# Kernel tuning notes

Measured on AMD Instinct MI355X. Metric: run time of the kernel, lower is better.

Reference implementation:

```python
import jax, jax.numpy as jnp
import numpy as np

N_NODES = 50000
D_IN = 128
D_OUT = 128
N_EDGES = 800000


def setup_inputs() -> dict:
    key = jax.random.key(0)
    ks = jax.random.split(key, 6)
    x = jax.random.normal(ks[0], (N_NODES, D_IN), dtype=jnp.float32)
    # xavier-uniform-ish init for the per-support weights
    limit = float(np.sqrt(6.0 / (D_IN + D_OUT)))
    weights = jax.random.uniform(ks[1], (2, D_IN, D_OUT), dtype=jnp.float32,
                                 minval=-limit, maxval=limit)
    edge_idx0 = jax.random.randint(ks[2], (2, N_EDGES), 0, N_NODES, dtype=jnp.int64 if jax.config.jax_enable_x64 else jnp.int32)
    vals0 = jax.random.uniform(ks[3], (N_EDGES,), dtype=jnp.float32)
    edge_idx1 = jax.random.randint(ks[4], (2, N_EDGES), 0, N_NODES, dtype=jnp.int64 if jax.config.jax_enable_x64 else jnp.int32)
    vals1 = jax.random.uniform(ks[5], (N_EDGES,), dtype=jnp.float32)
    return {"x": x, "weights": weights, "edge_idx0": edge_idx0, "vals0": vals0,
            "edge_idx1": edge_idx1, "vals1": vals1}


def _spmm(edge_idx, vals, dense, n_rows):
    # (sparse COO A) @ dense : out[row] += vals * dense[col]
    rows, cols = edge_idx[0], edge_idx[1]
    gathered = dense[cols] * vals[:, None]  # [E, D_OUT]
    return jax.ops.segment_sum(gathered, rows, num_segments=n_rows)


def reference(x, weights, edge_idx0, vals0, edge_idx1, vals1):
    n = x.shape[0]
    out = jnp.zeros((n, D_OUT), dtype=x.dtype)
    for w, ei, v in ((weights[0], edge_idx0, vals0), (weights[1], edge_idx1, vals1)):
        pre_sup = x @ w                       # [N, D_OUT] dense GEMM
        out = out + _spmm(ei, v, pre_sup, n)  # SpMM accumulate
    return jax.nn.relu(out)
```

## Files before the change

kernel.cpp:

```cpp
#include <hip/hip_runtime.h>

#define N_NODES 50000
#define D 128
#define N_EDGES 800000
#define SCAN_BLOCKS ((N_NODES + 255) / 256)
#define GEMM_BLOCKS ((N_NODES + 63) / 64)
#define BINS 196
#define NB1 64
#define CH1 12500
#define NKEY 2048

typedef __attribute__((ext_vector_type(8))) short short8;
typedef __attribute__((ext_vector_type(4))) float f32x4;
typedef __attribute__((ext_vector_type(2))) float f32x2;

__device__ __forceinline__ unsigned short f2bf(float f) {
    unsigned u = __builtin_bit_cast(unsigned, f);
    u += 0x7FFFu + ((u >> 16) & 1u);
    return (unsigned short)(u >> 16);
}
__device__ __forceinline__ float bflo(unsigned p) {
    return __builtin_bit_cast(float, p << 16);
}
__device__ __forceinline__ float bfhi(unsigned p) {
    return __builtin_bit_cast(float, p & 0xFFFF0000u);
}

__global__ __launch_bounds__(256) void wt_build(const float* __restrict__ w,
                                                unsigned short* __restrict__ wt) {
    int i = blockIdx.x * 256 + threadIdx.x;
    if (i < 2 * D * D) {
        int s = i >> 14, rem = i & 16383, c = rem >> 7, k = rem & 127;
        wt[i] = f2bf(w[s * D * D + k * D + c]);
    }
}

template<int NS>
__device__ __forceinline__ void gemm_body(const float* __restrict__ x,
                                          const unsigned short* __restrict__ wt,
                                          unsigned short* __restrict__ pre0,
                                          unsigned short* __restrict__ pre1,
                                          int n_rows, int blk) {
    const int lane = threadIdx.x & 63;
    const int wid  = threadIdx.x >> 6;
    const int q    = lane >> 4;
    const int rlo  = lane & 15;
    const int r0   = blk * 64 + wid * 16;
    if (r0 >= n_rows) return;

    const float4* x4 = (const float4*)x;
    int arow  = r0 + rlo;
    int arowc = arow < n_rows ? arow : n_rows - 1;

    short8 afr[4];
    #pragma unroll
    for (int kb = 0; kb < 4; ++kb) {
        float4 fa = x4[(size_t)arowc * 32 + kb * 8 + q * 2];
        float4 fb = x4[(size_t)arowc * 32 + kb * 8 + q * 2 + 1];
        short8 a;
        a[0] = (short)f2bf(fa.x); a[1] = (short)f2bf(fa.y);
        a[2] = (short)f2bf(fa.z); a[3] = (short)f2bf(fa.w);
        a[4] = (short)f2bf(fb.x); a[5] = (short)f2bf(fb.y);
        a[6] = (short)f2bf(fb.z); a[7] = (short)f2bf(fb.w);
        afr[kb] = a;
    }

    const short8* wt8 = (const short8*)wt;
    f32x4 acc[NS][8];
    #pragma unroll
    for (int s = 0; s < NS; ++s)
        #pragma unroll
        for (int t = 0; t < 8; ++t)
            acc[s][t] = (f32x4){0.f, 0.f, 0.f, 0.f};

    #pragma unroll
    for (int t = 0; t < 8; ++t) {
        int c = t * 16 + rlo;
        #pragma unroll
        for (int kb = 0; kb < 4; ++kb) {
            short8 b0 = wt8[(size_t)c * 16 + kb * 4 + q];
            acc[0][t] = __builtin_amdgcn_mfma_f32_16x16x32_bf16(afr[kb], b0, acc[0][t], 0, 0, 0);
            if (NS == 2) {
                short8 b1 = wt8[(size_t)(D + c) * 16 + kb * 4 + q];
                acc[NS - 1][t] = __builtin_amdgcn_mfma_f32_16x16x32_bf16(afr[kb], b1, acc[NS - 1][t], 0, 0, 0);
            }
        }
    }

    #pragma unroll
    for (int i = 0; i < 4; ++i) {
        int rw = r0 + q * 4 + i;
        if (rw < n_rows) {
            #pragma unroll
            for (int t = 0; t < 8; ++t) {
                pre0[(size_t)rw * D + t * 16 + rlo] = f2bf(acc[0][t][i]);
                if (NS == 2) pre1[(size_t)rw * D + t * 16 + rlo] = f2bf(acc[NS - 1][t][i]);
            }
        }
    }
}


__global__ __launch_bounds__(256) void p1_count(const int* __restrict__ r0,
                                                const int* __restrict__ r1,
                                                int* __restrict__ h) {
    int s = blockIdx.y, blk = blockIdx.x;
    const int* r = s ? r1 : r0;
    __shared__ int hist[BINS];
    for (int i = threadIdx.x; i < BINS; i += 256) hist[i] = 0;
    __syncthreads();
    int start = blk * CH1, end = start + CH1;
    for (int e = start + (int)threadIdx.x; e < end; e += 256)
        atomicAdd(&hist[r[e] >> 8], 1);
    __syncthreads();
    for (int i = threadIdx.x; i < BINS; i += 256)
        h[(size_t)(s * NB1 + blk) * BINS + i] = hist[i];
}

__global__ __launch_bounds__(256) void binredscan(const int* __restrict__ h,
                                                  int* __restrict__ binbase) {
    int s = blockIdx.x, t = threadIdx.x;
    int acc[8] = {0, 0, 0, 0, 0, 0, 0, 0};
    if (t < BINS) {
        for (int blk = 0; blk < NB1; blk += 8) {
            #pragma unroll
            for (int j = 0; j < 8; ++j)
                acc[j] += h[(size_t)(s * NB1 + blk + j) * BINS + t];
        }
    }
    int v = acc[0] + acc[1] + acc[2] + acc[3] + acc[4] + acc[5] + acc[6] + acc[7];
    const int lane = t & 63, wid = t >> 6;
    __shared__ int ws[4];
    int incl = v;
    #pragma unroll
    for (int o = 1; o < 64; o <<= 1) { int tv = __shfl_up(incl, o); if (lane >= o) incl += tv; }
    if (lane == 63) ws[wid] = incl;
    __syncthreads();
    int wbase = 0;
    #pragma unroll
    for (int j = 0; j < 4; ++j) wbase += (j < wid) ? ws[j] : 0;
    int excl = wbase + incl - v;
    if (t < BINS) binbase[s * (BINS + 1) + t] = excl;
    if (t == BINS - 1) binbase[s * (BINS + 1) + BINS] = excl + v;
}

__global__ __launch_bounds__(64) void blkscan(int* __restrict__ h,
                                              const int* __restrict__ binbase) {
    int s = blockIdx.y, bin = blockIdx.x, t = threadIdx.x;
    size_t idx = (size_t)(s * NB1 + t) * BINS + bin;
    int v = h[idx];
    int incl = v;
    #pragma unroll
    for (int o = 1; o < 64; o <<= 1) { int tv = __shfl_up(incl, o); if (t >= o) incl += tv; }
    h[idx] = binbase[s * (BINS + 1) + bin] + (incl - v);
}

#define LWT_STRIDE 17
__global__ __launch_bounds__(256) void k_fill_gemm(const float* __restrict__ x,
                                                   const unsigned short* __restrict__ wt,
                                                   unsigned short* __restrict__ pre0,
                                                   unsigned short* __restrict__ pre1,
                                                   const int* __restrict__ r0, const int* __restrict__ c0,
                                                   const float* __restrict__ v0,
                                                   const int* __restrict__ r1, const int* __restrict__ c1,
                                                   const float* __restrict__ v1,
                                                   const int* __restrict__ h,
                                                   int2* __restrict__ rec, int n_rows) {
    __shared__ int base[BINS];
    __shared__ int cnt2[BINS];
    __shared__ short8 lwt[2 * D * LWT_STRIDE];
    int bid = blockIdx.x;
    if (bid < 2 * NB1) {
        int s = bid & 1, blk = bid >> 1;
        const int*   r = s ? r1 : r0;
        const int*   c = s ? c1 : c0;
        const float* v = s ? v1 : v0;
        int2* rs = rec + (size_t)s * N_EDGES;
        for (int i = threadIdx.x; i < BINS; i += 256) {
            base[i] = h[(size_t)(s * NB1 + blk) * BINS + i];
            cnt2[i] = 0;
        }
        __syncthreads();
        int start = blk * CH1, end = start + CH1;
        for (int e = start + (int)threadIdx.x; e < end; e += 256) {
            int rr = r[e], cc = c[e];
            float vv = v[e];
            int bin = rr >> 8;
            int lr = atomicAdd(&cnt2[bin], 1);
            rs[base[bin] + lr] = make_int2((cc << 8) | (rr & 255), __float_as_int(vv));
        }
    } else {
        int blk = bid - 2 * NB1;
        const short8* wg = (const short8*)wt;
        for (int i = threadIdx.x; i < 2 * D * 16; i += 256) {
            int cc = i >> 4, ee = i & 15;
            lwt[cc * LWT_STRIDE + ee] = wg[i];
        }
        __syncthreads();

        const int lane = threadIdx.x & 63;
        const int wid  = threadIdx.x >> 6;
        const int q    = lane >> 4;
        const int rlo  = lane & 15;
        const int r0g  = blk * 64 + wid * 16;
        if (r0g < n_rows) {
            const float4* x4 = (const float4*)x;
            int arow  = r0g + rlo;
            int arowc = arow < n_rows ? arow : n_rows - 1;

            short8 afr[4];
            #pragma unroll
            for (int kb = 0; kb < 4; ++kb) {
                float4 fa = x4[(size_t)arowc * 32 + kb * 8 + q * 2];
                float4 fb = x4[(size_t)arowc * 32 + kb * 8 + q * 2 + 1];
                short8 a;
                a[0] = (short)f2bf(fa.x); a[1] = (short)f2bf(fa.y);
                a[2] = (short)f2bf(fa.z); a[3] = (short)f2bf(fa.w);
                a[4] = (short)f2bf(fb.x); a[5] = (short)f2bf(fb.y);
                a[6] = (short)f2bf(fb.z); a[7] = (short)f2bf(fb.w);
                afr[kb] = a;
            }

            f32x4 acc[2][8];
            #pragma unroll
            for (int s = 0; s < 2; ++s)
                #pragma unroll
                for (int t = 0; t < 8; ++t)
                    acc[s][t] = (f32x4){0.f, 0.f, 0.f, 0.f};

            #pragma unroll
            for (int t = 0; t < 8; ++t) {
                int c = t * 16 + rlo;
                #pragma unroll
                for (int kb = 0; kb < 4; ++kb) {
                    short8 b0 = lwt[c * LWT_STRIDE + kb * 4 + q];
                    acc[0][t] = __builtin_amdgcn_mfma_f32_16x16x32_bf16(afr[kb], b0, acc[0][t], 0, 0, 0);
                    short8 b1 = lwt[(D + c) * LWT_STRIDE + kb * 4 + q];
                    acc[1][t] = __builtin_amdgcn_mfma_f32_16x16x32_bf16(afr[kb], b1, acc[1][t], 0, 0, 0);
                }
            }

            #pragma unroll
            for (int i = 0; i < 4; ++i) {
                int rw = r0g + q * 4 + i;
                if (rw < n_rows) {
                    #pragma unroll
                    for (int t = 0; t < 8; ++t) {
                        pre0[(size_t)rw * D + t * 16 + rlo] = f2bf(acc[0][t][i]);
                        pre1[(size_t)rw * D + t * 16 + rlo] = f2bf(acc[1][t][i]);
                    }
                }
            }
        }
    }
}

__global__ __launch_bounds__(512) void p2_sort(const int* __restrict__ binbase,
                                               const int2* __restrict__ rec,
                                               unsigned* __restrict__ ep,
                                               int* __restrict__ off) {
    int s = blockIdx.y, bin = blockIdx.x, t = threadIdx.x;
    int bs  = binbase[s * (BINS + 1) + bin];
    int be  = binbase[s * (BINS + 1) + bin + 1];
    int cnt = be - bs;
    const int2* rs = rec + (size_t)s * N_EDGES;
    unsigned* es = ep + (size_t)s * N_EDGES;
    __shared__ int lc[NKEY];
    __shared__ int cur[NKEY];
    __shared__ int ws[8];
    #pragma unroll
    for (int j = 0; j < NKEY / 512; ++j) lc[t + j * 512] = 0;
    __syncthreads();
    for (int i = t; i < cnt; i += 512) {
        int2 R = rs[bs + i];
        int col = R.x >> 8;
        int key = ((R.x & 255) << 3) | (col >> 13);
        atomicAdd(&lc[key], 1);
    }
    __syncthreads();
    int kb = t * 4;
    int s0 = lc[kb], s1 = lc[kb + 1], s2 = lc[kb + 2], s3 = lc[kb + 3];
    int tot = s0 + s1 + s2 + s3;
    const int lane = t & 63, wid = t >> 6;
    int incl = tot;
    #pragma unroll
    for (int o = 1; o < 64; o <<= 1) { int tv = __shfl_up(incl, o); if (lane >= o) incl += tv; }
    if (lane == 63) ws[wid] = incl;
    __syncthreads();
    int wbase = 0;
    #pragma unroll
    for (int j = 0; j < 8; ++j) wbase += (j < wid) ? ws[j] : 0;
    int excl = wbase + incl - tot;
    cur[kb]     = excl;
    cur[kb + 1] = excl + s0;
    cur[kb + 2] = excl + s0 + s1;
    cur[kb + 3] = excl + s0 + s1 + s2;
    if ((t & 1) == 0) {
        int row = bin * 256 + (t >> 1);
        if (row < N_NODES) off[s * (N_NODES + 1) + row] = bs + excl;
    }
    if (bin == 0 && t == 0) off[s * (N_NODES + 1) + N_NODES] = N_EDGES;
    __syncthreads();
    for (int i = t; i < cnt; i += 512) {
        int2 R = rs[bs + i];
        int col = R.x >> 8;
        int key = ((R.x & 255) << 3) | (col >> 13);
        int p = atomicAdd(&cur[key], 1);
        es[bs + p] = ((unsigned)col << 16) | (unsigned)f2bf(__int_as_float(R.y));
    }
}

__device__ __forceinline__ void row_acc4(const unsigned* __restrict__ ep,
                                         const unsigned* __restrict__ prew,
                                         int b, int e, int lane, float& ax, float& ay) {
    int i = b;
    for (; i + 7 < e; i += 8) {
        unsigned E[8], P[8];
        #pragma unroll
        for (int j = 0; j < 8; ++j) E[j] = ep[i + j];
        #pragma unroll
        for (int j = 0; j < 8; ++j) P[j] = prew[(size_t)(E[j] >> 16) * 64 + lane];
        #pragma unroll
        for (int j = 0; j < 8; ++j) {
            float w = bflo(E[j]);
            ax = fmaf(w, bflo(P[j]), ax);
            ay = fmaf(w, bfhi(P[j]), ay);
        }
    }
    if (i + 3 < e) {
        unsigned E[4], P[4];
        #pragma unroll
        for (int j = 0; j < 4; ++j) E[j] = ep[i + j];
        #pragma unroll
        for (int j = 0; j < 4; ++j) P[j] = prew[(size_t)(E[j] >> 16) * 64 + lane];
        #pragma unroll
        for (int j = 0; j < 4; ++j) {
            float w = bflo(E[j]);
            ax = fmaf(w, bflo(P[j]), ax);
            ay = fmaf(w, bfhi(P[j]), ay);
        }
        i += 4;
    }
    for (; i < e; ++i) {
        unsigned E = ep[i];
        float w = bflo(E);
        unsigned p = prew[(size_t)(E >> 16) * 64 + lane];
        ax = fmaf(w, bflo(p), ax);
        ay = fmaf(w, bfhi(p), ay);
    }
}

__global__ __launch_bounds__(256) void gather_fused4(const int* __restrict__ off_base,
                                                     const unsigned* __restrict__ ep_base,
                                                     const unsigned short* __restrict__ pre0,
                                                     const unsigned short* __restrict__ pre1,
                                                     float* __restrict__ out, int n_rows) {
    const int lane = threadIdx.x & 63;
    const int wid  = threadIdx.x >> 6;
    const int wpg  = 4 * gridDim.x;
    const unsigned* ep1b = ep_base + N_EDGES;
    const int* o1 = off_base + (N_NODES + 1);
    const unsigned* pre0w = (const unsigned*)pre0;
    const unsigned* pre1w = (const unsigned*)pre1;
    f32x2* out2 = (f32x2*)out;
    for (int r = blockIdx.x * 4 + wid; r < n_rows; r += wpg) {
        float ax0 = 0.f, ay0 = 0.f, ax1 = 0.f, ay1 = 0.f;
        int i0 = __builtin_amdgcn_readfirstlane(off_base[r]);
        int e0 = __builtin_amdgcn_readfirstlane(off_base[r + 1]);
        int i1 = __builtin_amdgcn_readfirstlane(o1[r]);
        int e1 = __builtin_amdgcn_readfirstlane(o1[r + 1]);
        while (i0 + 7 < e0 && i1 + 7 < e1) {
            unsigned E0[8], E1[8], P0[8], P1[8];
            #pragma unroll
            for (int j = 0; j < 8; ++j) { E0[j] = ep_base[i0 + j]; E1[j] = ep1b[i1 + j]; }
            #pragma unroll
            for (int j = 0; j < 8; ++j) {
                P0[j] = pre0w[(size_t)(E0[j] >> 16) * 64 + lane];
                P1[j] = pre1w[(size_t)(E1[j] >> 16) * 64 + lane];
            }
            #pragma unroll
            for (int j = 0; j < 8; ++j) {
                float w0 = bflo(E0[j]);
                float w1 = bflo(E1[j]);
                ax0 = fmaf(w0, bflo(P0[j]), ax0);
                ay0 = fmaf(w0, bfhi(P0[j]), ay0);
                ax1 = fmaf(w1, bflo(P1[j]), ax1);
                ay1 = fmaf(w1, bfhi(P1[j]), ay1);
            }
            i0 += 8; i1 += 8;
        }
        row_acc4(ep_base, pre0w, i0, e0, lane, ax0, ay0);
        row_acc4(ep1b,    pre1w, i1, e1, lane, ax1, ay1);
        f32x2 o;
        o.x = fmaxf(ax0 + ax1, 0.f);
        o.y = fmaxf(ay0 + ay1, 0.f);
        __builtin_nontemporal_store(o, &out2[(size_t)r * 64 + lane]);
    }
}

__device__ __forceinline__ void row_acc(const int2* __restrict__ ep,
                                        const unsigned short* __restrict__ pre,
                                        int b, int e, int lane, float& ax, float& ay) {
    int i = b;
    for (; i + 7 < e; i += 8) {
        int2 E[8];
        unsigned P[8];
        #pragma unroll
        for (int j = 0; j < 8; ++j) E[j] = ep[i + j];
        #pragma unroll
        for (int j = 0; j < 8; ++j) P[j] = *(const unsigned*)(pre + (size_t)E[j].x * D + 2 * lane);
        #pragma unroll
        for (int j = 0; j < 8; ++j) {
            float w = __int_as_float(E[j].y);
            ax = fmaf(w, bflo(P[j]), ax);
            ay = fmaf(w, bfhi(P[j]), ay);
        }
    }
    for (; i < e; ++i) {
        int2 e0 = ep[i];
        float w = __int_as_float(e0.y);
        unsigned p = *(const unsigned*)(pre + (size_t)e0.x * D + 2 * lane);
        ax = fmaf(w, bflo(p), ax);
        ay = fmaf(w, bfhi(p), ay);
    }
}

__global__ __launch_bounds__(256) void gather_fused(const int* __restrict__ off_base,
                                                    const int2* __restrict__ ep_base,
                                                    const unsigned short* __restrict__ pre0,
                                                    const unsigned short* __restrict__ pre1,
                                                    float* __restrict__ out, int n_rows) {
    const int lane = threadIdx.x & 63;
    const int wid  = threadIdx.x >> 6;
    const int wpg  = 4 * gridDim.x;
    const int2* ep1b = ep_base + N_EDGES;
    const int* o1 = off_base + (N_NODES + 1);
    float2* out2 = (float2*)out;
    for (int r = blockIdx.x * 4 + wid; r < n_rows; r += wpg) {
        float ax0 = 0.f, ay0 = 0.f, ax1 = 0.f, ay1 = 0.f;
        row_acc(ep_base, pre0, off_base[r], off_base[r + 1], lane, ax0, ay0);
        row_acc(ep1b,    pre1, o1[r], o1[r + 1], lane, ax1, ay1);
        float2 o;
        o.x = fmaxf(ax0 + ax1, 0.f);
        o.y = fmaxf(ay0 + ay1, 0.f);
        out2[(size_t)r * 64 + lane] = o;
    }
}

__global__ __launch_bounds__(256) void gemm_mfma2(const float* __restrict__ x,
                                                  const unsigned short* __restrict__ wt,
                                                  unsigned short* __restrict__ pre0,
                                                  unsigned short* __restrict__ pre1, int n_rows) {
    gemm_body<2>(x, wt, pre0, pre1, n_rows, blockIdx.x);
}
__global__ __launch_bounds__(256) void gemm_mfma1(const float* __restrict__ x,
                                                  const unsigned short* __restrict__ wt,
                                                  unsigned short* __restrict__ pre, int n_rows) {
    gemm_body<1>(x, wt, pre, pre, n_rows, blockIdx.x);
}

__global__ __launch_bounds__(256) void hist_rank(const int* __restrict__ r0,
                                                 const int* __restrict__ r1,
                                                 int* __restrict__ cnt_base,
                                                 int* __restrict__ rank_base, int n_edges) {
    int s = blockIdx.y;
    const int* r = s ? r1 : r0;
    int* cnt  = cnt_base + s * N_NODES;
    int* rank = rank_base + (size_t)s * N_EDGES;
    for (int e = blockIdx.x * 256 + threadIdx.x; e < n_edges; e += gridDim.x * 256)
        rank[e] = atomicAdd(&cnt[r[e]], 1);
}

__global__ __launch_bounds__(256) void scanA(const int* __restrict__ cnt_base,
                                             int* __restrict__ bsum) {
    int s = blockIdx.y;
    int i = blockIdx.x * 256 + threadIdx.x;
    int v = (i < N_NODES) ? cnt_base[s * N_NODES + i] : 0;
    const int lane = threadIdx.x & 63;
    const int wid  = threadIdx.x >> 6;
    __shared__ int ws[4];
    #pragma unroll
    for (int off = 32; off > 0; off >>= 1) v += __shfl_down(v, off);
    if (lane == 0) ws[wid] = v;
    __syncthreads();
    if (threadIdx.x == 0)
        bsum[s * SCAN_BLOCKS + blockIdx.x] = ws[0] + ws[1] + ws[2] + ws[3];
}

__global__ __launch_bounds__(256) void scanC2(const int* __restrict__ cnt_base,
                                              const int* __restrict__ bsum,
                                              int* __restrict__ off_base) {
    int s = blockIdx.y;
    int t = threadIdx.x;
    const int lane = t & 63;
    const int wid  = t >> 6;
    __shared__ int ws[4];
    __shared__ int base_s;
    int bv = (t < (int)blockIdx.x && t < SCAN_BLOCKS) ? bsum[s * SCAN_BLOCKS + t] : 0;
    #pragma unroll
    for (int off = 32; off > 0; off >>= 1) bv += __shfl_down(bv, off);
    if (lane == 0) ws[wid] = bv;
    __syncthreads();
    if (t == 0) base_s = ws[0] + ws[1] + ws[2] + ws[3];
    __syncthreads();
    int base = base_s;
    __syncthreads();
    int i = blockIdx.x * 256 + t;
    int v = (i < N_NODES) ? cnt_base[s * N_NODES + i] : 0;
    int incl = v;
    #pragma unroll
    for (int off = 1; off < 64; off <<= 1) {
        int tv = __shfl_up(incl, off);
        if (lane >= off) incl += tv;
    }
    if (lane == 63) ws[wid] = incl;
    __syncthreads();
    int wbase = 0;
    #pragma unroll
    for (int j = 0; j < 4; ++j) wbase += (j < wid) ? ws[j] : 0;
    int* off = off_base + s * (N_NODES + 1);
    if (i < N_NODES)
        off[i] = base + wbase + incl - v;
    if (blockIdx.x == 0 && t == 0)
        off[N_NODES] = N_EDGES;
}

__global__ __launch_bounds__(256) void scatter_csr(const int* __restrict__ r0, const int* __restrict__ c0,
                                                   const float* __restrict__ v0,
                                                   const int* __restrict__ r1, const int* __restrict__ c1,
                                                   const float* __restrict__ v1,
                                                   const int* __restrict__ off_base,
                                                   const int* __restrict__ rank_base,
                                                   int2* __restrict__ ep_base, int n_edges) {
    int s = blockIdx.y;
    const int*   r    = s ? r1 : r0;
    const int*   c    = s ? c1 : c0;
    const float* v    = s ? v1 : v0;
    const int*   off  = off_base + s * (N_NODES + 1);
    const int*   rank = rank_base + (size_t)s * N_EDGES;
    int2* ep = ep_base + (size_t)s * N_EDGES;
    for (int e = blockIdx.x * 256 + threadIdx.x; e < n_edges; e += gridDim.x * 256) {
        int p = off[r[e]] + rank[e];
        int2 rec;
        rec.x = c[e];
        rec.y = __float_as_int(v[e]);
        ep[p] = rec;
    }
}

template<int ACCUM_RELU>
__global__ __launch_bounds__(256) void gather_one(const int* __restrict__ off,
                                                  const int2* __restrict__ ep,
                                                  const unsigned short* __restrict__ pre,
                                                  float* __restrict__ out, int n_rows) {
    const int lane = threadIdx.x & 63;
    const int wid  = threadIdx.x >> 6;
    const int wpg  = 4 * gridDim.x;
    float2* out2 = (float2*)out;
    for (int r = blockIdx.x * 4 + wid; r < n_rows; r += wpg) {
        float ax = 0.f, ay = 0.f;
        row_acc(ep, pre, off[r], off[r + 1], lane, ax, ay);
        float2 o;
        if (ACCUM_RELU) {
            float2 prev = out2[(size_t)r * 64 + lane];
            o.x = fmaxf(prev.x + ax, 0.f);
            o.y = fmaxf(prev.y + ay, 0.f);
        } else {
            o.x = ax; o.y = ay;
        }
        out2[(size_t)r * 64 + lane] = o;
    }
}

extern "C" void kernel_launch(void* const* d_in, const int* in_sizes, int n_in,
                              void* d_out, int out_size, void* d_ws, size_t ws_size,
                              hipStream_t stream) {
    const float* x       = (const float*)d_in[0];
    const float* weights = (const float*)d_in[1];
    const int*   ei0     = (const int*)d_in[2];
    const float* v0      = (const float*)d_in[3];
    const int*   ei1     = (const int*)d_in[4];
    const float* v1      = (const float*)d_in[5];
    float* out = (float*)d_out;

    dim3 blk(256);
    const size_t PRE_B = (size_t)N_NODES * D * sizeof(unsigned short);
    const size_t WT_B  = (size_t)2 * D * D * sizeof(unsigned short);
    const size_t H_B   = (size_t)2 * NB1 * BINS * 4;
    const size_t BB_B  = (size_t)2 * (BINS + 1) * 4;
    const size_t OFF_B = (size_t)2 * (N_NODES + 1) * 4;
    const size_t E8    = (size_t)2 * N_EDGES * sizeof(int2);
    const size_t E4    = (size_t)2 * N_EDGES * 4;

    char* wsb = (char*)d_ws;
    size_t needNew = 2 * PRE_B + WT_B + H_B + BB_B + OFF_B + E8 + E4;
    size_t needA1 = 2 * PRE_B + WT_B
                  + (size_t)(2 * (N_NODES + 1) + 2 * N_NODES + 2 * SCAN_BLOCKS) * 4
                  + E8 + (size_t)2 * N_EDGES * 4;

    if (ws_size >= needNew) {
        unsigned short* pre0 = (unsigned short*)wsb;
        unsigned short* pre1 = (unsigned short*)(wsb + PRE_B);
        unsigned short* wt   = (unsigned short*)(wsb + 2 * PRE_B);
        int*  h       = (int*)(wsb + 2 * PRE_B + WT_B);
        int*  binbase = (int*)((char*)h + H_B);
        int*  off     = (int*)((char*)binbase + BB_B);
        int2* rec     = (int2*)((char*)off + OFF_B);
        unsigned* ep  = (unsigned*)(rec + (size_t)2 * N_EDGES);

        wt_build<<<128, blk, 0, stream>>>(weights, wt);
        p1_count<<<dim3(NB1, 2), blk, 0, stream>>>(ei0, ei1, h);
        binredscan<<<2, blk, 0, stream>>>(h, binbase);
        blkscan<<<dim3(BINS, 2), dim3(64), 0, stream>>>(h, binbase);
        k_fill_gemm<<<2 * NB1 + GEMM_BLOCKS, blk, 0, stream>>>(
            x, wt, pre0, pre1,
            ei0, ei0 + N_EDGES, v0, ei1, ei1 + N_EDGES, v1,
            h, rec, N_NODES);
        p2_sort<<<dim3(BINS, 2), dim3(512), 0, stream>>>(binbase, rec, ep, off);
        gather_fused4<<<12500, blk, 0, stream>>>(off, ep, pre0, pre1, out, N_NODES);
    } else if (ws_size >= needA1) {
        unsigned short* pre0 = (unsigned short*)wsb;
        unsigned short* pre1 = (unsigned short*)(wsb + PRE_B);
        unsigned short* wt   = (unsigned short*)(wsb + 2 * PRE_B);
        int*  off  = (int*)(wsb + 2 * PRE_B + WT_B);
        int*  cnt  = off + 2 * (N_NODES + 1);
        int*  bsum = cnt + 2 * N_NODES;
        int2* ep   = (int2*)(bsum + 2 * SCAN_BLOCKS);
        int*  rank = (int*)(ep + (size_t)2 * N_EDGES);

        hipMemsetAsync(cnt, 0, (size_t)2 * N_NODES * sizeof(int), stream);
        wt_build<<<128, blk, 0, stream>>>(weights, wt);
        hist_rank<<<dim3(1024, 2), blk, 0, stream>>>(ei0, ei1, cnt, rank, N_EDGES);
        gemm_mfma2<<<GEMM_BLOCKS, blk, 0, stream>>>(x, wt, pre0, pre1, N_NODES);
        scanA<<<dim3(SCAN_BLOCKS, 2), blk, 0, stream>>>(cnt, bsum);
        scanC2<<<dim3(SCAN_BLOCKS, 2), blk, 0, stream>>>(cnt, bsum, off);
        scatter_csr<<<dim3(1024, 2), blk, 0, stream>>>(ei0, ei0 + N_EDGES, v0,
                                                       ei1, ei1 + N_EDGES, v1,
                                                       off, rank, ep, N_EDGES);
        gather_fused<<<12500, blk, 0, stream>>>(off, ep, pre0, pre1, out, N_NODES);
    } else {
        unsigned short* pre = (unsigned short*)wsb;
        unsigned short* wt  = (unsigned short*)(wsb + PRE_B);
        int*  off  = (int*)(wsb + PRE_B + WT_B);
        int*  cnt  = off + (N_NODES + 1);
        int*  bsum = cnt + N_NODES;
        int2* ep   = (int2*)(bsum + SCAN_BLOCKS);
        int*  rank = (int*)pre;

        wt_build<<<128, blk, 0, stream>>>(weights, wt);
        const int* rows[2] = {ei0, ei1};
        const int* cols[2] = {ei0 + N_EDGES, ei1 + N_EDGES};
        const float* vals[2] = {v0, v1};
        for (int s = 0; s < 2; ++s) {
            hipMemsetAsync(cnt, 0, (size_t)N_NODES * sizeof(int), stream);
            hist_rank<<<dim3(1024, 1), blk, 0, stream>>>(rows[s], rows[s], cnt, rank, N_EDGES);
            scanA<<<dim3(SCAN_BLOCKS, 1), blk, 0, stream>>>(cnt, bsum);
            scanC2<<<dim3(SCAN_BLOCKS, 1), blk, 0, stream>>>(cnt, bsum, off);
            scatter_csr<<<dim3(1024, 1), blk, 0, stream>>>(rows[s], cols[s], vals[s],
                                                           rows[s], cols[s], vals[s],
                                                           off, rank, ep, N_EDGES);
            gemm_mfma1<<<GEMM_BLOCKS, blk, 0, stream>>>(x, wt + (size_t)s * D * D, pre, N_NODES);
            if (s == 0)
                gather_one<0><<<12500, blk, 0, stream>>>(off, ep, pre, out, N_NODES);
            else
                gather_one<1><<<12500, blk, 0, stream>>>(off, ep, pre, out, N_NODES);
        }
    }
}
```

Before: 123.1 us.

## Fuse weight conversion into count kernel and halve GEMM LDS footprint

Merges the weight transpose/bf16 conversion into the histogram-count kernel so one launch does both, removing a kernel launch. The fused fill+GEMM kernel now stages one support's weights at a time into LDS (half the shared memory), computes that support, then reloads the second, aiming for higher occupancy of the GEMM/fill blocks. The cost is an extra LDS reload and barrier per block and two passes over the MFMA loop instead of one interleaved pass.

```diff
diff --git a/kernel.cpp b/kernel.cpp
--- a/kernel.cpp
+++ b/kernel.cpp
@@ -9,6 +9,7 @@
 #define NB1 64
 #define CH1 12500
 #define NKEY 2048
+#define WTB 128
 
 typedef __attribute__((ext_vector_type(8))) short short8;
 typedef __attribute__((ext_vector_type(4))) float f32x4;
@@ -24,15 +25,6 @@
 }
 __device__ __forceinline__ float bfhi(unsigned p) {
     return __builtin_bit_cast(float, p & 0xFFFF0000u);
-}
-
-__global__ __launch_bounds__(256) void wt_build(const float* __restrict__ w,
-                                                unsigned short* __restrict__ wt) {
-    int i = blockIdx.x * 256 + threadIdx.x;
-    if (i < 2 * D * D) {
-        int s = i >> 14, rem = i & 16383, c = rem >> 7, k = rem & 127;
-        wt[i] = f2bf(w[s * D * D + k * D + c]);
-    }
 }
 
 template<int NS>
@@ -101,20 +93,31 @@
 }
 
 
-__global__ __launch_bounds__(256) void p1_count(const int* __restrict__ r0,
-                                                const int* __restrict__ r1,
-                                                int* __restrict__ h) {
-    int s = blockIdx.y, blk = blockIdx.x;
-    const int* r = s ? r1 : r0;
-    __shared__ int hist[BINS];
-    for (int i = threadIdx.x; i < BINS; i += 256) hist[i] = 0;
-    __syncthreads();
-    int start = blk * CH1, end = start + CH1;
-    for (int e = start + (int)threadIdx.x; e < end; e += 256)
-        atomicAdd(&hist[r[e] >> 8], 1);
-    __syncthreads();
-    for (int i = threadIdx.x; i < BINS; i += 256)
-        h[(size_t)(s * NB1 + blk) * BINS + i] = hist[i];
+__global__ __launch_bounds__(256) void p1_count_wt(const int* __restrict__ r0,
+                                                   const int* __restrict__ r1,
+                                                   int* __restrict__ h,
+                                                   const float* __restrict__ w,
+                                                   unsigned short* __restrict__ wt) {
+    int bid = blockIdx.x;
+    if (bid < 2 * NB1) {
+        int s = bid & 1, blk = bid >> 1;
+        const int* r = s ? r1 : r0;
+        __shared__ int hist[BINS];
+        for (int i = threadIdx.x; i < BINS; i += 256) hist[i] = 0;
+        __syncthreads();
+        int start = blk * CH1, end = start + CH1;
+        for (int e = start + (int)threadIdx.x; e < end; e += 256)
+            atomicAdd(&hist[r[e] >> 8], 1);
+        __syncthreads();
+        for (int i = threadIdx.x; i < BINS; i += 256)
+            h[(size_t)(s * NB1 + blk) * BINS + i] = hist[i];
+    } else {
+        int i = (bid - 2 * NB1) * 256 + threadIdx.x;
+        if (i < 2 * D * D) {
+            int s = i >> 14, rem = i & 16383, c = rem >> 7, k = rem & 127;
+            wt[i] = f2bf(w[s * D * D + k * D + c]);
+        }
+    }
 }
 
 __global__ __launch_bounds__(256) void binredscan(const int* __restrict__ h,
@@ -168,7 +171,7 @@
                                                    int2* __restrict__ rec, int n_rows) {
     __shared__ int base[BINS];
     __shared__ int cnt2[BINS];
-    __shared__ short8 lwt[2 * D * LWT_STRIDE];
+    __shared__ short8 lwt[D * LWT_STRIDE];
     int bid = blockIdx.x;
     if (bid < 2 * NB1) {
         int s = bid & 1, blk = bid >> 1;
@@ -191,24 +194,17 @@
         }
     } else {
         int blk = bid - 2 * NB1;
-        const short8* wg = (const short8*)wt;
-        for (int i = threadIdx.x; i < 2 * D * 16; i += 256) {
-            int cc = i >> 4, ee = i & 15;
-            lwt[cc * LWT_STRIDE + ee] = wg[i];
-        }
-        __syncthreads();
-
         const int lane = threadIdx.x & 63;
         const int wid  = threadIdx.x >> 6;
         const int q    = lane >> 4;
         const int rlo  = lane & 15;
         const int r0g  = blk * 64 + wid * 16;
-        if (r0g < n_rows) {
-            const float4* x4 = (const float4*)x;
+        const float4* x4 = (const float4*)x;
+
+        short8 afr[4];
+        {
             int arow  = r0g + rlo;
-            int arowc = arow < n_rows ? arow : n_rows - 1;
-
-            short8 afr[4];
+            int arowc = arow < n_rows ? (arow < 0 ? 0 : arow) : n_rows - 1;
             #pragma unroll
             for (int kb = 0; kb < 4; ++kb) {
                 float4 fa = x4[(size_t)arowc * 32 + kb * 8 + q * 2];
@@ -220,34 +216,39 @@
                 a[6] = (short)f2bf(fb.z); a[7] = (short)f2bf(fb.w);
                 afr[kb] = a;
             }
-
-            f32x4 acc[2][8];
-            #pragma unroll
-            for (int s = 0; s < 2; ++s)
+        }
+
+        #pragma unroll
+        for (int s = 0; s < 2; ++s) {
+            const short8* wg = (const short8*)wt + (size_t)s * D * 16;
+            if (s) __syncthreads();
+            for (int i = threadIdx.x; i < D * 16; i += 256) {
+                int cc = i >> 4, ee = i & 15;
+                lwt[cc * LWT_STRIDE + ee] = wg[i];
+            }
+            __syncthreads();
+
+            if (r0g < n_rows) {
+                f32x4 acc[8];
                 #pragma unroll
-                for (int t = 0; t < 8; ++t)
-                    acc[s][t] = (f32x4){0.f, 0.f, 0.f, 0.f};
-
-            #pragma unroll
-            for (int t = 0; t < 8; ++t) {
-                int c = t * 16 + rlo;
+                for (int t = 0; t < 8; ++t) acc[t] = (f32x4){0.f, 0.f, 0.f, 0.f};
                 #pragma unroll
-                for (int kb = 0; kb < 4; ++kb) {
-                    short8 b0 = lwt[c * LWT_STRIDE + kb * 4 + q];
-                    acc[0][t] = __builtin_amdgcn_mfma_f32_16x16x32_bf16(afr[kb], b0, acc[0][t], 0, 0, 0);
-                    short8 b1 = lwt[(D + c) * LWT_STRIDE + kb * 4 + q];
-                    acc[1][t] = __builtin_amdgcn_mfma_f32_16x16x32_bf16(afr[kb], b1, acc[1][t], 0, 0, 0);
+                for (int t = 0; t < 8; ++t) {
+                    int c = t * 16 + rlo;
+                    #pragma unroll
+                    for (int kb = 0; kb < 4; ++kb) {
+                        short8 b = lwt[c * LWT_STRIDE + kb * 4 + q];
+                        acc[t] = __builtin_amdgcn_mfma_f32_16x16x32_bf16(afr[kb], b, acc[t], 0, 0, 0);
+                    }
                 }
-            }
-
-            #pragma unroll
-            for (int i = 0; i < 4; ++i) {
-                int rw = r0g + q * 4 + i;
-                if (rw < n_rows) {
-                    #pragma unroll
-                    for (int t = 0; t < 8; ++t) {
-                        pre0[(size_t)rw * D + t * 16 + rlo] = f2bf(acc[0][t][i]);
-                        pre1[(size_t)rw * D + t * 16 + rlo] = f2bf(acc[1][t][i]);
+                unsigned short* pre = s ? pre1 : pre0;
+                #pragma unroll
+                for (int i = 0; i < 4; ++i) {
+                    int rw = r0g + q * 4 + i;
+                    if (rw < n_rows) {
+                        #pragma unroll
+                        for (int t = 0; t < 8; ++t)
+                            pre[(size_t)rw * D + t * 16 + rlo] = f2bf(acc[t][i]);
                     }
                 }
             }
@@ -398,6 +399,15 @@
     }
 }
 
+__global__ __launch_bounds__(256) void wt_build(const float* __restrict__ w,
+                                                unsigned short* __restrict__ wt) {
+    int i = blockIdx.x * 256 + threadIdx.x;
+    if (i < 2 * D * D) {
+        int s = i >> 14, rem = i & 16383, c = rem >> 7, k = rem & 127;
+        wt[i] = f2bf(w[s * D * D + k * D + c]);
+    }
+}
+
 __device__ __forceinline__ void row_acc(const int2* __restrict__ ep,
                                         const unsigned short* __restrict__ pre,
                                         int b, int e, int lane, float& ax, float& ay) {
@@ -608,8 +618,7 @@
         int2* rec     = (int2*)((char*)off + OFF_B);
         unsigned* ep  = (unsigned*)(rec + (size_t)2 * N_EDGES);
 
-        wt_build<<<128, blk, 0, stream>>>(weights, wt);
-        p1_count<<<dim3(NB1, 2), blk, 0, stream>>>(ei0, ei1, h);
+        p1_count_wt<<<2 * NB1 + WTB, blk, 0, stream>>>(ei0, ei1, h, weights, wt);
         binredscan<<<2, blk, 0, stream>>>(h, binbase);
         blkscan<<<dim3(BINS, 2), dim3(64), 0, stream>>>(h, binbase);
         k_fill_gemm<<<2 * NB1 + GEMM_BLOCKS, blk, 0, stream>>>(
```

New measurement: 119.9 us, median of 2. 2.6% less time.
